# Performance work log

Hardware: AMD Instinct MI355X
Metric: run time of the kernel (lower is better)

Reference implementation:

```python
import jax, jax.numpy as jnp
import numpy as np

N_NODES = 100000
N_EDGES = 1600000
FEAT = 128
HID = 128
N_GRAPHS = 128


def setup_inputs() -> dict:
    key = jax.random.key(0)
    ks = jax.random.split(key, 20)
    inp = {
        'x': jax.random.normal(ks[0], (N_NODES, FEAT), dtype=jnp.float32),
        'edge_index': jax.random.randint(ks[1], (2, N_EDGES), 0, N_NODES, dtype=jnp.int32),
        'batch': jnp.sort(jax.random.randint(ks[2], (N_NODES,), 0, N_GRAPHS, dtype=jnp.int32)),
        'layer_K': 1,
    }
    # Xavier-uniform weights, zero biases (matches LinearPrune.reset_parameters)
    i = 3
    for l in range(3):
        in_dim = FEAT if l == 0 else HID
        lim1 = float(np.sqrt(6.0 / (in_dim + HID)))
        lim2 = float(np.sqrt(6.0 / (HID + HID)))
        inp[f'W1_l{l}'] = jax.random.uniform(ks[i], (HID, in_dim), jnp.float32, -lim1, lim1); i += 1
        inp[f'b1_l{l}'] = jnp.zeros((HID,), jnp.float32)
        inp[f'W2_l{l}'] = jax.random.uniform(ks[i], (HID, HID), jnp.float32, -lim2, lim2); i += 1
        inp[f'b2_l{l}'] = jnp.zeros((HID,), jnp.float32)
    return inp


def _gin_conv(x, src, dst, W1, b1, W2, b2, k):
    # GINConvPrune.forward with skip=1, eps=0, prune=False
    out = x
    for _ in range(k):  # k = layer_K, static int (deterministic finetune/eval path)
        # propagate: gather neighbor feats then scatter-add at dst nodes
        agg = jax.ops.segment_sum(out[src], dst, num_segments=x.shape[0])
        out = (out + agg) * 0.5
    if k == 0:
        out = jax.ops.segment_sum(x[src], dst, num_segments=x.shape[0])
    out = out + x  # (1 + eps) * x_r with eps = 0
    h = jax.nn.relu(out @ W1.T + b1)
    return h @ W2.T + b2


def reference(x, edge_index, batch, layer_K,
              W1_l0, b1_l0, W2_l0, b2_l0,
              W1_l1, b1_l1, W2_l1, b2_l1,
              W1_l2, b1_l2, W2_l2, b2_l2):
    src, dst = edge_index[0], edge_index[1]
    params = [(W1_l0, b1_l0, W2_l0, b2_l0),
              (W1_l1, b1_l1, W2_l1, b2_l1),
              (W1_l2, b1_l2, W2_l2, b2_l2)]
    k = int(layer_K)
    h = x
    pooled = []
    for (W1, b1, W2, b2) in params:
        h = _gin_conv(h, src, dst, W1, b1, W2, b2, k)
        h = jax.nn.relu(h)  # outer self.act
        pooled.append(jax.ops.segment_sum(h, batch, num_segments=N_GRAPHS))  # global_add_pool
    return jnp.concatenate(pooled, axis=1)  # [G, 3*HID]
```

## Files before the change

kernel.cpp:

```cpp
#include <hip/hip_runtime.h>

#define NN 100000
#define NE 1600000
#define FEAT 128
#define NGRAPH 128
#define BSHIFT 9
#define NB 196
#define NCHUNK 400
#define CHUNK 4000

typedef __attribute__((ext_vector_type(8))) short bf16x8;
typedef __attribute__((ext_vector_type(4))) float f32x4;
typedef __attribute__((ext_vector_type(4))) unsigned u32x4;

union U4 { u32x4 u; bf16x8 v; };

__device__ __forceinline__ unsigned short f2bf(float f) {
    unsigned u = __float_as_uint(f);
    return (unsigned short)((u + 0x7fffu + ((u >> 16) & 1u)) >> 16);
}
__device__ __forceinline__ float bf2f(unsigned short h) {
    return __uint_as_float(((unsigned)h) << 16);
}
__device__ __forceinline__ unsigned packbf(float f) {
    unsigned short h = f2bf(f);
    return (unsigned)h | ((unsigned)f2bf(f - bf2f(h)) << 16);
}
__device__ __forceinline__ uint2 unpack2(unsigned p0, unsigned p1) {
    return make_uint2((p0 & 0xffffu) | (p1 << 16), (p0 >> 16) | (p1 & 0xffff0000u));
}
__device__ __forceinline__ void unpack8(u32x4 a, u32x4 b, bf16x8& hv, bf16x8& lv) {
    uint2 r0 = unpack2(a.x, a.y), r1 = unpack2(a.z, a.w);
    uint2 r2 = unpack2(b.x, b.y), r3 = unpack2(b.z, b.w);
    U4 h, l;
    h.u = (u32x4){r0.x, r1.x, r2.x, r3.x};
    l.u = (u32x4){r0.y, r1.y, r2.y, r3.y};
    hv = h.v; lv = l.v;
}

__global__ __launch_bounds__(256)
void wsplit_frag_kernel(const float* __restrict__ W, short* __restrict__ Wf)
{
    int i = blockIdx.x * 256 + threadIdx.x;
    int o = i >> 7, k = i & 127;
    float f = W[i];
    unsigned short h = f2bf(f);
    short lo = (short)f2bf(f - bf2f(h));
    int ct = o >> 4, lr = o & 15, kc = k >> 5, q = (k >> 3) & 3, j = k & 7;
    int idx = (kc * 8 + ct) * 512 + ((q << 4) | lr) * 8 + j;
    Wf[idx] = (short)h;
    Wf[16384 + idx] = lo;
}

__global__ __launch_bounds__(256)
void p1a_count(const int* __restrict__ ei, int* __restrict__ cnt_T)
{
    __shared__ int hist[NB];
    const int b = blockIdx.x, tid = threadIdx.x;
    for (int i = tid; i < NB; i += 256) hist[i] = 0;
    __syncthreads();
    const int e0 = b * CHUNK;
    for (int e = e0 + tid; e < e0 + CHUNK; e += 256)
        atomicAdd(&hist[ei[NE + e] >> BSHIFT], 1);
    __syncthreads();
    for (int k = tid; k < NB; k += 256) cnt_T[k * NCHUNK + b] = hist[k];
}

__global__ __launch_bounds__(1024)
void scan1_kernel(const int* __restrict__ in, int* __restrict__ out,
                  int* __restrict__ bsum, int n)
{
    __shared__ int sh[1024];
    const int tid = threadIdx.x;
    const int gid = blockIdx.x * 1024 + tid;
    int v = (gid < n) ? in[gid] : 0;
    sh[tid] = v;
    __syncthreads();
    #pragma unroll
    for (int d = 1; d < 1024; d <<= 1) {
        int t = (tid >= d) ? sh[tid - d] : 0;
        __syncthreads();
        sh[tid] += t;
        __syncthreads();
    }
    if (gid < n) out[gid] = sh[tid] - v;
    if (tid == 1023) bsum[blockIdx.x] = sh[1023];
}

__global__ __launch_bounds__(128)
void scan2_kernel(int* __restrict__ bsum, int nb)
{
    __shared__ int sh[128];
    const int tid = threadIdx.x;
    int v = (tid < nb) ? bsum[tid] : 0;
    sh[tid] = v;
    __syncthreads();
    #pragma unroll
    for (int d = 1; d < 128; d <<= 1) {
        int t = (tid >= d) ? sh[tid - d] : 0;
        __syncthreads();
        sh[tid] += t;
        __syncthreads();
    }
    if (tid < nb) bsum[tid] = sh[tid] - v;
}

__global__ __launch_bounds__(1024)
void scan3g_kernel(int* __restrict__ arr, const int* __restrict__ bsum, int n)
{
    const int gid = blockIdx.x * 1024 + threadIdx.x;
    if (gid < n) arr[gid] += bsum[blockIdx.x];
}

__global__ __launch_bounds__(256)
void p1b_scatter(const int* __restrict__ ei, const int* __restrict__ offs_T,
                 int2* __restrict__ ebuf)
{
    __shared__ int cur[NB];
    const int b = blockIdx.x, tid = threadIdx.x;
    for (int i = tid; i < NB; i += 256) cur[i] = offs_T[i * NCHUNK + b];
    __syncthreads();
    const int e0 = b * CHUNK;
    for (int e = e0 + tid; e < e0 + CHUNK; e += 256) {
        int s = ei[e], d = ei[NE + e];
        int pos = atomicAdd(&cur[d >> BSHIFT], 1);
        ebuf[pos] = make_int2(s, d);
    }
}

__global__ __launch_bounds__(512)
void p2_csr(const int2* __restrict__ ebuf, const int* __restrict__ offs_T,
            int* __restrict__ off, int* __restrict__ csr)
{
    __shared__ int degc[512];
    __shared__ int sh[512];
    const int k = blockIdx.x, tid = threadIdx.x;
    const int base = k << BSHIFT;
    const int bs = offs_T[k * NCHUNK];
    const int be = (k == NB - 1) ? NE : offs_T[(k + 1) * NCHUNK];
    degc[tid] = 0;
    __syncthreads();
    for (int e = bs + tid; e < be; e += 512)
        atomicAdd(&degc[ebuf[e].y - base], 1);
    __syncthreads();
    int v = degc[tid];
    sh[tid] = v;
    __syncthreads();
    #pragma unroll
    for (int d = 1; d < 512; d <<= 1) {
        int t = (tid >= d) ? sh[tid - d] : 0;
        __syncthreads();
        sh[tid] += t;
        __syncthreads();
    }
    const int excl = bs + sh[tid] - v;
    const int n = base + tid;
    if (n <= NN) off[n] = excl;
    degc[tid] = excl;
    __syncthreads();
    for (int e = bs + tid; e < be; e += 512) {
        int2 p = ebuf[e];
        int slot = atomicAdd(&degc[p.y - base], 1);
        csr[slot] = p.x;
    }
}

__global__ __launch_bounds__(256)
void aggregate_pack_kernel(const float* __restrict__ h, const int* __restrict__ off,
                           const int* __restrict__ csr, unsigned* __restrict__ xP, int nn)
{
    const int node = blockIdx.x * 4 + (threadIdx.x >> 6);
    if (node >= nn) return;
    const int lane = threadIdx.x & 63;
    const int s = off[node], e = off[node + 1];
    float2 acc = make_float2(0.f, 0.f);
    for (int base = s; base < e; base += 64) {
        const int cnt = min(64, e - base);
        int src_l = (base + lane < e) ? csr[base + lane] : 0;
        for (int jb = 0; jb < cnt; jb += 16) {
            float2 v[16];
            #pragma unroll
            for (int q = 0; q < 16; ++q) {
                int sq = __shfl(src_l, (jb + q) & 63);
                v[q] = reinterpret_cast<const float2*>(h + (size_t)sq * FEAT)[lane];
            }
            #pragma unroll
            for (int q = 0; q < 16; ++q) {
                if (jb + q < cnt) { acc.x += v[q].x; acc.y += v[q].y; }
            }
        }
    }
    float2 hv = reinterpret_cast<const float2*>(h + (size_t)node * FEAT)[lane];
    float ox = (hv.x + acc.x) * 0.5f + hv.x;
    float oy = (hv.y + acc.y) * 0.5f + hv.y;
    uint2 pw = make_uint2(packbf(ox), packbf(oy));
    *reinterpret_cast<uint2*>(&xP[(size_t)node * FEAT + lane * 2]) = pw;
}

__global__ __launch_bounds__(512, 4)
void layer_fused_kernel(const unsigned* __restrict__ aP, const short* __restrict__ Wf1,
                        const short* __restrict__ Wf2, const float* __restrict__ b1,
                        const float* __restrict__ b2, float* __restrict__ outC, int n_nodes)
{
    __shared__ short wlds[32768];
    const int tid = threadIdx.x;
    const int lane = tid & 63;
    const int w = tid >> 6;
    const int lr = lane & 15;
    const int lq = lane >> 4;
    const int n0 = blockIdx.x * 128 + w * 16 + lr;
    const bool v0 = (n0 < n_nodes);
    const size_t rb0 = (size_t)n0 * FEAT + lq * 8;
    u32x4 zz = {};

    {
        const bf16x8* src = reinterpret_cast<const bf16x8*>(Wf1);
        bf16x8* dst = reinterpret_cast<bf16x8*>(wlds);
        #pragma unroll
        for (int it = 0; it < 8; ++it)
            dst[it * 512 + tid] = src[it * 512 + tid];
    }
    u32x4 paa = v0 ? *reinterpret_cast<const u32x4*>(&aP[rb0])     : zz;
    u32x4 pab = v0 ? *reinterpret_cast<const u32x4*>(&aP[rb0 + 4]) : zz;
    __syncthreads();

    f32x4 acc[8] = {};
    bf16x8 ah, al;
    unpack8(paa, pab, ah, al);
    #pragma unroll
    for (int kc = 0; kc < 4; ++kc) {
        u32x4 na = zz, nb = zz;
        if (kc < 3) {
            const int ko = (kc + 1) * 32;
            na = v0 ? *reinterpret_cast<const u32x4*>(&aP[rb0 + ko])     : zz;
            nb = v0 ? *reinterpret_cast<const u32x4*>(&aP[rb0 + ko + 4]) : zz;
        }
        #pragma unroll
        for (int ct = 0; ct < 8; ++ct) {
            const int ra = (kc * 8 + ct) * 512 + lane * 8;
            bf16x8 bh = *reinterpret_cast<const bf16x8*>(&wlds[ra]);
            bf16x8 bl = *reinterpret_cast<const bf16x8*>(&wlds[16384 + ra]);
            acc[ct] = __builtin_amdgcn_mfma_f32_16x16x32_bf16(bh, ah, acc[ct], 0, 0, 0);
            acc[ct] = __builtin_amdgcn_mfma_f32_16x16x32_bf16(bh, al, acc[ct], 0, 0, 0);
            acc[ct] = __builtin_amdgcn_mfma_f32_16x16x32_bf16(bl, ah, acc[ct], 0, 0, 0);
        }
        if (kc < 3) unpack8(na, nb, ah, al);
    }

    unsigned h1p[32];
    #pragma unroll
    for (int ct = 0; ct < 8; ++ct) {
        const int c0 = ct * 16 + lq * 4;
        float4 bv = *reinterpret_cast<const float4*>(&b1[c0]);
        h1p[ct * 4 + 0] = packbf(fmaxf(acc[ct][0] + bv.x, 0.f));
        h1p[ct * 4 + 1] = packbf(fmaxf(acc[ct][1] + bv.y, 0.f));
        h1p[ct * 4 + 2] = packbf(fmaxf(acc[ct][2] + bv.z, 0.f));
        h1p[ct * 4 + 3] = packbf(fmaxf(acc[ct][3] + bv.w, 0.f));
    }

    __syncthreads();
    {
        const bf16x8* src = reinterpret_cast<const bf16x8*>(Wf2);
        bf16x8* dst = reinterpret_cast<bf16x8*>(wlds);
        #pragma unroll
        for (int it = 0; it < 8; ++it)
            dst[it * 512 + tid] = src[it * 512 + tid];
    }
    __syncthreads();

    f32x4 acc2[8] = {};
    const int aown = (lq & 1) * 2;
    const bool hi_t = (lq & 2) != 0;
    #pragma unroll
    for (int kc = 0; kc < 4; ++kc) {
        unsigned pd[8];
        #pragma unroll
        for (int m = 0; m < 4; ++m) {
            unsigned vA = h1p[(2 * kc) * 4 + m];
            unsigned vB = h1p[(2 * kc + 1) * 4 + m];
            unsigned sA0 = __shfl(vA, lr + 16 * aown);
            unsigned sB0 = __shfl(vB, lr + 16 * aown);
            unsigned sA1 = __shfl(vA, lr + 16 * (aown + 1));
            unsigned sB1 = __shfl(vB, lr + 16 * (aown + 1));
            pd[m]     = hi_t ? sB0 : sA0;
            pd[4 + m] = hi_t ? sB1 : sA1;
        }
        u32x4 qa = {pd[0], pd[1], pd[2], pd[3]};
        u32x4 qb = {pd[4], pd[5], pd[6], pd[7]};
        bf16x8 hh, hl;
        unpack8(qa, qb, hh, hl);
        #pragma unroll
        for (int ct = 0; ct < 8; ++ct) {
            const int ra = (kc * 8 + ct) * 512 + lane * 8;
            bf16x8 bh = *reinterpret_cast<const bf16x8*>(&wlds[ra]);
            bf16x8 bl = *reinterpret_cast<const bf16x8*>(&wlds[16384 + ra]);
            acc2[ct] = __builtin_amdgcn_mfma_f32_16x16x32_bf16(bh, hh, acc2[ct], 0, 0, 0);
            acc2[ct] = __builtin_amdgcn_mfma_f32_16x16x32_bf16(bh, hl, acc2[ct], 0, 0, 0);
            acc2[ct] = __builtin_amdgcn_mfma_f32_16x16x32_bf16(bl, hh, acc2[ct], 0, 0, 0);
        }
    }

    if (v0) {
        #pragma unroll
        for (int ct = 0; ct < 8; ++ct) {
            const int c0 = ct * 16 + lq * 4;
            float4 bv = *reinterpret_cast<const float4*>(&b2[c0]);
            float4 o;
            o.x = fmaxf(acc2[ct][0] + bv.x, 0.f);
            o.y = fmaxf(acc2[ct][1] + bv.y, 0.f);
            o.z = fmaxf(acc2[ct][2] + bv.z, 0.f);
            o.w = fmaxf(acc2[ct][3] + bv.w, 0.f);
            *reinterpret_cast<float4*>(&outC[(size_t)n0 * FEAT + c0]) = o;
        }
    }
}

__global__ __launch_bounds__(512)
void pool_kernel(const float* __restrict__ y, const int* __restrict__ batch,
                 float* __restrict__ out, int n_nodes, int layer)
{
    const int g = blockIdx.x;
    int lo = 0, hi = n_nodes;
    while (lo < hi) { int mid = (lo + hi) >> 1; if (batch[mid] < g) lo = mid + 1; else hi = mid; }
    const int start = lo;
    hi = n_nodes;
    while (lo < hi) { int mid = (lo + hi) >> 1; if (batch[mid] < g + 1) lo = mid + 1; else hi = mid; }
    const int end = lo;

    const int tid = threadIdx.x;
    const int f = tid & 127;
    const int q = tid >> 7;
    float sum = 0.f;
    for (int n = start + q; n < end; n += 4)
        sum += y[(size_t)n * FEAT + f];

    __shared__ float red[512];
    red[tid] = sum;
    __syncthreads();
    if (tid < 128)
        out[g * (3 * FEAT) + layer * FEAT + tid]
            = red[tid] + red[tid + 128] + red[tid + 256] + red[tid + 384];
}

__global__ __launch_bounds__(256)
void scatter_kernel(const float* __restrict__ h, const int* __restrict__ ei,
                    float* __restrict__ agg, int n_edges)
{
    int e = blockIdx.x * 4 + (threadIdx.x >> 6);
    if (e >= n_edges) return;
    int lane = threadIdx.x & 63;
    int s = ei[e];
    int d = ei[n_edges + e];
    float2 v = reinterpret_cast<const float2*>(h + (size_t)s * FEAT)[lane];
    float* ap = agg + (size_t)d * FEAT + lane * 2;
    atomicAdd(ap, v.x);
    atomicAdd(ap + 1, v.y);
}

__global__ __launch_bounds__(256)
void combine_kernel(const float* __restrict__ h, float* __restrict__ agg_xeff, size_t n4)
{
    size_t i = (size_t)blockIdx.x * 256 + threadIdx.x;
    if (i >= n4) return;
    float4 a = reinterpret_cast<const float4*>(h)[i];
    float4 g = reinterpret_cast<float4*>(agg_xeff)[i];
    float4 o;
    o.x = (a.x + g.x) * 0.5f + a.x;
    o.y = (a.y + g.y) * 0.5f + a.y;
    o.z = (a.z + g.z) * 0.5f + a.z;
    o.w = (a.w + g.w) * 0.5f + a.w;
    reinterpret_cast<float4*>(agg_xeff)[i] = o;
}

__global__ __launch_bounds__(256, 2)
void gemm_relu_kernel(const float* __restrict__ A, const float* __restrict__ W,
                      const float* __restrict__ bias, float* __restrict__ out, int n_nodes)
{
    __shared__ float xt[64][128];
    __shared__ float wt[64][128];
    const int tid = threadIdx.x;
    const int row0 = blockIdx.x * 128;
    const int r  = tid >> 1;
    const int ks = (tid & 1) << 5;
    const int tn = (tid >> 4) << 3;
    const int to = (tid & 15) << 3;
    float acc[8][8] = {};

    for (int c = 0; c < 2; ++c) {
        const int k0 = c * 64;
        {
            const float4* wrow = reinterpret_cast<const float4*>(W + r * FEAT + k0 + ks);
            #pragma unroll
            for (int i = 0; i < 8; ++i) {
                float4 w4 = wrow[i];
                int kk = ks + i * 4;
                wt[kk + 0][r] = w4.x; wt[kk + 1][r] = w4.y;
                wt[kk + 2][r] = w4.z; wt[kk + 3][r] = w4.w;
            }
        }
        {
            const int n = row0 + r;
            if (n < n_nodes) {
                const float4* ar = reinterpret_cast<const float4*>(A + (size_t)n * FEAT + k0 + ks);
                #pragma unroll
                for (int i = 0; i < 8; ++i) {
                    float4 a4 = ar[i];
                    int kk = ks + i * 4;
                    xt[kk + 0][r] = a4.x; xt[kk + 1][r] = a4.y;
                    xt[kk + 2][r] = a4.z; xt[kk + 3][r] = a4.w;
                }
            } else {
                #pragma unroll
                for (int i = 0; i < 8; ++i) {
                    int kk = ks + i * 4;
                    xt[kk + 0][r] = 0.f; xt[kk + 1][r] = 0.f;
                    xt[kk + 2][r] = 0.f; xt[kk + 3][r] = 0.f;
                }
            }
        }
        __syncthreads();
        #pragma unroll 4
        for (int k = 0; k < 64; ++k) {
            float4 x0 = *reinterpret_cast<const float4*>(&xt[k][tn]);
            float4 x1 = *reinterpret_cast<const float4*>(&xt[k][tn + 4]);
            float4 w0 = *reinterpret_cast<const float4*>(&wt[k][to]);
            float4 w1 = *reinterpret_cast<const float4*>(&wt[k][to + 4]);
            float xv[8] = {x0.x, x0.y, x0.z, x0.w, x1.x, x1.y, x1.z, x1.w};
            float wv[8] = {w0.x, w0.y, w0.z, w0.w, w1.x, w1.y, w1.z, w1.w};
            #pragma unroll
            for (int i = 0; i < 8; ++i)
                #pragma unroll
                for (int j = 0; j < 8; ++j)
                    acc[i][j] = fmaf(xv[i], wv[j], acc[i][j]);
        }
        __syncthreads();
    }

    float bv[8];
    #pragma unroll
    for (int j = 0; j < 8; ++j) bv[j] = bias[to + j];
    #pragma unroll
    for (int i = 0; i < 8; ++i) {
        int n = row0 + tn + i;
        if (n >= n_nodes) break;
        float4 o0, o1;
        o0.x = fmaxf(acc[i][0] + bv[0], 0.f);
        o0.y = fmaxf(acc[i][1] + bv[1], 0.f);
        o0.z = fmaxf(acc[i][2] + bv[2], 0.f);
        o0.w = fmaxf(acc[i][3] + bv[3], 0.f);
        o1.x = fmaxf(acc[i][4] + bv[4], 0.f);
        o1.y = fmaxf(acc[i][5] + bv[5], 0.f);
        o1.z = fmaxf(acc[i][6] + bv[6], 0.f);
        o1.w = fmaxf(acc[i][7] + bv[7], 0.f);
        float* op = out + (size_t)n * FEAT + to;
        *reinterpret_cast<float4*>(op) = o0;
        *reinterpret_cast<float4*>(op + 4) = o1;
    }
}

extern "C" void kernel_launch(void* const* d_in, const int* in_sizes, int n_in,
                              void* d_out, int out_size, void* d_ws, size_t ws_size,
                              hipStream_t stream)
{
    const float* x     = (const float*)d_in[0];
    const int*   ei    = (const int*)d_in[1];
    const int*   batch = (const int*)d_in[2];
    const float* W1[3] = {(const float*)d_in[4], (const float*)d_in[8],  (const float*)d_in[12]};
    const float* b1[3] = {(const float*)d_in[5], (const float*)d_in[9],  (const float*)d_in[13]};
    const float* W2[3] = {(const float*)d_in[6], (const float*)d_in[10], (const float*)d_in[14]};
    const float* b2[3] = {(const float*)d_in[7], (const float*)d_in[11], (const float*)d_in[15]};

    const size_t nf = (size_t)NN * FEAT;
    float* outp = (float*)d_out;
    const int fused_grid = (NN + 127) / 128;
    const int M = NB * NCHUNK;
    const int scanM_blocks = (M + 1023) / 1024;
    const int WN = FEAT * FEAT;

    const size_t need_full = 2 * nf * 4 + (size_t)(NN + 1 + NE) * 4 + (size_t)12 * WN * 2;

    if (ws_size >= need_full) {
        unsigned* xeffP = (unsigned*)d_ws;
        float* bufC     = (float*)(xeffP + nf);
        int* off        = (int*)(bufC + nf);
        int* csr        = off + (NN + 1);
        short* wbase    = (short*)(csr + NE);
        short* wf[6];
        for (int i = 0; i < 6; ++i) wf[i] = wbase + (size_t)i * 2 * WN;
        int* cnt_T  = (int*)xeffP;
        int* offs_T = cnt_T + M;
        int* bsum   = offs_T + M;
        int2* ebuf  = (int2*)bufC;

        const float* Ws[6] = {W1[0], W2[0], W1[1], W2[1], W1[2], W2[2]};
        for (int i = 0; i < 6; ++i)
            wsplit_frag_kernel<<<WN / 256, 256, 0, stream>>>(Ws[i], wf[i]);

        p1a_count<<<NCHUNK, 256, 0, stream>>>(ei, cnt_T);
        scan1_kernel<<<scanM_blocks, 1024, 0, stream>>>(cnt_T, offs_T, bsum, M);
        scan2_kernel<<<1, 128, 0, stream>>>(bsum, scanM_blocks);
        scan3g_kernel<<<scanM_blocks, 1024, 0, stream>>>(offs_T, bsum, M);
        p1b_scatter<<<NCHUNK, 256, 0, stream>>>(ei, offs_T, ebuf);
        p2_csr<<<NB, 512, 0, stream>>>(ebuf, offs_T, off, csr);

        const float* h = x;
        for (int l = 0; l < 3; ++l) {
            aggregate_pack_kernel<<<(NN + 3) / 4, 256, 0, stream>>>(h, off, csr, xeffP, NN);
            layer_fused_kernel<<<fused_grid, 512, 0, stream>>>(xeffP, wf[2 * l], wf[2 * l + 1],
                                                               b1[l], b2[l], bufC, NN);
            pool_kernel<<<NGRAPH, 512, 0, stream>>>(bufC, batch, outp, NN, l);
            h = bufC;
        }
    } else if (ws_size >= 3 * nf * 4) {
        float* bufA = (float*)d_ws;
        float* bufB = bufA + nf;
        float* bufC = bufB + nf;
        const int gg = (NN + 127) / 128;
        const float* h = x;
        for (int l = 0; l < 3; ++l) {
            hipMemsetAsync(bufA, 0, nf * 4, stream);
            scatter_kernel<<<(NE + 3) / 4, 256, 0, stream>>>(h, ei, bufA, NE);
            combine_kernel<<<(int)((nf / 4 + 255) / 256), 256, 0, stream>>>(h, bufA, nf / 4);
            gemm_relu_kernel<<<gg, 256, 0, stream>>>(bufA, W1[l], b1[l], bufB, NN);
            gemm_relu_kernel<<<gg, 256, 0, stream>>>(bufB, W2[l], b2[l], bufC, NN);
            pool_kernel<<<NGRAPH, 512, 0, stream>>>(bufC, batch, outp, NN, l);
            h = bufC;
        }
    }
}
```

Baseline: 692.2 us.

## Fuse neighbor aggregation into the per-layer MLP kernel with ping-pong output buffers

Removes the separate aggregation kernel and does the CSR gather-sum inside the fused MLP kernel. Each wave aggregates its 16 rows one after another and shuffles the bf16-packed results straight into the MFMA A-operand registers. This drops the intermediate bf16 write and read and one launch per layer. Because the kernel now reads h while writing its output, the output alternates between two buffers, and the workspace layout moves to fit them. The cost is that each wave handles its 16 rows' gathers serially with fewer waves in flight (512-thread blocks at 128 rows each), which may hurt latency hiding for the memory-bound gather.

```diff
diff --git a/kernel.cpp b/kernel.cpp
--- a/kernel.cpp
+++ b/kernel.cpp
@@ -165,42 +165,12 @@
     }
 }
 
-__global__ __launch_bounds__(256)
-void aggregate_pack_kernel(const float* __restrict__ h, const int* __restrict__ off,
-                           const int* __restrict__ csr, unsigned* __restrict__ xP, int nn)
-{
-    const int node = blockIdx.x * 4 + (threadIdx.x >> 6);
-    if (node >= nn) return;
-    const int lane = threadIdx.x & 63;
-    const int s = off[node], e = off[node + 1];
-    float2 acc = make_float2(0.f, 0.f);
-    for (int base = s; base < e; base += 64) {
-        const int cnt = min(64, e - base);
-        int src_l = (base + lane < e) ? csr[base + lane] : 0;
-        for (int jb = 0; jb < cnt; jb += 16) {
-            float2 v[16];
-            #pragma unroll
-            for (int q = 0; q < 16; ++q) {
-                int sq = __shfl(src_l, (jb + q) & 63);
-                v[q] = reinterpret_cast<const float2*>(h + (size_t)sq * FEAT)[lane];
-            }
-            #pragma unroll
-            for (int q = 0; q < 16; ++q) {
-                if (jb + q < cnt) { acc.x += v[q].x; acc.y += v[q].y; }
-            }
-        }
-    }
-    float2 hv = reinterpret_cast<const float2*>(h + (size_t)node * FEAT)[lane];
-    float ox = (hv.x + acc.x) * 0.5f + hv.x;
-    float oy = (hv.y + acc.y) * 0.5f + hv.y;
-    uint2 pw = make_uint2(packbf(ox), packbf(oy));
-    *reinterpret_cast<uint2*>(&xP[(size_t)node * FEAT + lane * 2]) = pw;
-}
-
 __global__ __launch_bounds__(512, 4)
-void layer_fused_kernel(const unsigned* __restrict__ aP, const short* __restrict__ Wf1,
-                        const short* __restrict__ Wf2, const float* __restrict__ b1,
-                        const float* __restrict__ b2, float* __restrict__ outC, int n_nodes)
+void layer_mega_kernel(const float* __restrict__ h, const int* __restrict__ off,
+                       const int* __restrict__ csr,
+                       const short* __restrict__ Wf1, const short* __restrict__ Wf2,
+                       const float* __restrict__ b1, const float* __restrict__ b2,
+                       float* __restrict__ outC, int n_nodes)
 {
     __shared__ short wlds[32768];
     const int tid = threadIdx.x;
@@ -208,10 +178,7 @@
     const int w = tid >> 6;
     const int lr = lane & 15;
     const int lq = lane >> 4;
-    const int n0 = blockIdx.x * 128 + w * 16 + lr;
-    const bool v0 = (n0 < n_nodes);
-    const size_t rb0 = (size_t)n0 * FEAT + lq * 8;
-    u32x4 zz = {};
+    const int rowbase = blockIdx.x * 128 + w * 16;
 
     {
         const bf16x8* src = reinterpret_cast<const bf16x8*>(Wf1);
@@ -220,31 +187,66 @@
         for (int it = 0; it < 8; ++it)
             dst[it * 512 + tid] = src[it * 512 + tid];
     }
-    u32x4 paa = v0 ? *reinterpret_cast<const u32x4*>(&aP[rb0])     : zz;
-    u32x4 pab = v0 ? *reinterpret_cast<const u32x4*>(&aP[rb0 + 4]) : zz;
-    __syncthreads();
-
-    f32x4 acc[8] = {};
-    bf16x8 ah, al;
-    unpack8(paa, pab, ah, al);
+
+    unsigned areg[32] = {};
+    #pragma unroll
+    for (int r = 0; r < 16; ++r) {
+        const int row = rowbase + r;
+        float2 acc = make_float2(0.f, 0.f);
+        if (row < n_nodes) {
+            const int s = off[row], e = off[row + 1];
+            for (int base = s; base < e; base += 64) {
+                const int cnt = min(64, e - base);
+                int src_l = (base + lane < e) ? csr[base + lane] : 0;
+                for (int jb = 0; jb < cnt; jb += 16) {
+                    float2 v[16];
+                    #pragma unroll
+                    for (int q = 0; q < 16; ++q) {
+                        int sq = __shfl(src_l, (jb + q) & 63);
+                        v[q] = reinterpret_cast<const float2*>(h + (size_t)sq * FEAT)[lane];
+                    }
+                    #pragma unroll
+                    for (int q = 0; q < 16; ++q)
+                        if (jb + q < cnt) { acc.x += v[q].x; acc.y += v[q].y; }
+                }
+            }
+            float2 hv = reinterpret_cast<const float2*>(h + (size_t)row * FEAT)[lane];
+            acc.x = (hv.x + acc.x) * 0.5f + hv.x;
+            acc.y = (hv.y + acc.y) * 0.5f + hv.y;
+        }
+        unsigned px = packbf(acc.x), py = packbf(acc.y);
+        #pragma unroll
+        for (int kc = 0; kc < 4; ++kc) {
+            #pragma unroll
+            for (int t = 0; t < 4; ++t) {
+                const int srcl = kc * 16 + lq * 4 + t;
+                unsigned sx = __shfl(px, srcl);
+                unsigned sy = __shfl(py, srcl);
+                if (lr == r) {
+                    areg[kc * 8 + 2 * t]     = sx;
+                    areg[kc * 8 + 2 * t + 1] = sy;
+                }
+            }
+        }
+    }
+    __syncthreads();
+
+    f32x4 acc1[8] = {};
     #pragma unroll
     for (int kc = 0; kc < 4; ++kc) {
-        u32x4 na = zz, nb = zz;
-        if (kc < 3) {
-            const int ko = (kc + 1) * 32;
-            na = v0 ? *reinterpret_cast<const u32x4*>(&aP[rb0 + ko])     : zz;
-            nb = v0 ? *reinterpret_cast<const u32x4*>(&aP[rb0 + ko + 4]) : zz;
-        }
+        u32x4 qa = {areg[kc * 8 + 0], areg[kc * 8 + 1], areg[kc * 8 + 2], areg[kc * 8 + 3]};
+        u32x4 qb = {areg[kc * 8 + 4], areg[kc * 8 + 5], areg[kc * 8 + 6], areg[kc * 8 + 7]};
+        bf16x8 ah, al;
+        unpack8(qa, qb, ah, al);
         #pragma unroll
         for (int ct = 0; ct < 8; ++ct) {
             const int ra = (kc * 8 + ct) * 512 + lane * 8;
             bf16x8 bh = *reinterpret_cast<const bf16x8*>(&wlds[ra]);
             bf16x8 bl = *reinterpret_cast<const bf16x8*>(&wlds[16384 + ra]);
-            acc[ct] = __builtin_amdgcn_mfma_f32_16x16x32_bf16(bh, ah, acc[ct], 0, 0, 0);
-            acc[ct] = __builtin_amdgcn_mfma_f32_16x16x32_bf16(bh, al, acc[ct], 0, 0, 0);
-            acc[ct] = __builtin_amdgcn_mfma_f32_16x16x32_bf16(bl, ah, acc[ct], 0, 0, 0);
-        }
-        if (kc < 3) unpack8(na, nb, ah, al);
+            acc1[ct] = __builtin_amdgcn_mfma_f32_16x16x32_bf16(bh, ah, acc1[ct], 0, 0, 0);
+            acc1[ct] = __builtin_amdgcn_mfma_f32_16x16x32_bf16(bh, al, acc1[ct], 0, 0, 0);
+            acc1[ct] = __builtin_amdgcn_mfma_f32_16x16x32_bf16(bl, ah, acc1[ct], 0, 0, 0);
+        }
     }
 
     unsigned h1p[32];
@@ -252,10 +254,10 @@
     for (int ct = 0; ct < 8; ++ct) {
         const int c0 = ct * 16 + lq * 4;
         float4 bv = *reinterpret_cast<const float4*>(&b1[c0]);
-        h1p[ct * 4 + 0] = packbf(fmaxf(acc[ct][0] + bv.x, 0.f));
-        h1p[ct * 4 + 1] = packbf(fmaxf(acc[ct][1] + bv.y, 0.f));
-        h1p[ct * 4 + 2] = packbf(fmaxf(acc[ct][2] + bv.z, 0.f));
-        h1p[ct * 4 + 3] = packbf(fmaxf(acc[ct][3] + bv.w, 0.f));
+        h1p[ct * 4 + 0] = packbf(fmaxf(acc1[ct][0] + bv.x, 0.f));
+        h1p[ct * 4 + 1] = packbf(fmaxf(acc1[ct][1] + bv.y, 0.f));
+        h1p[ct * 4 + 2] = packbf(fmaxf(acc1[ct][2] + bv.z, 0.f));
+        h1p[ct * 4 + 3] = packbf(fmaxf(acc1[ct][3] + bv.w, 0.f));
     }
 
     __syncthreads();
@@ -300,7 +302,8 @@
         }
     }
 
-    if (v0) {
+    const int n0 = rowbase + lr;
+    if (n0 < n_nodes) {
         #pragma unroll
         for (int ct = 0; ct < 8; ++ct) {
             const int c0 = ct * 16 + lq * 4;
@@ -472,7 +475,7 @@
 
     const size_t nf = (size_t)NN * FEAT;
     float* outp = (float*)d_out;
-    const int fused_grid = (NN + 127) / 128;
+    const int mega_grid = (NN + 127) / 128;
     const int M = NB * NCHUNK;
     const int scanM_blocks = (M + 1023) / 1024;
     const int WN = FEAT * FEAT;
@@ -480,17 +483,17 @@
     const size_t need_full = 2 * nf * 4 + (size_t)(NN + 1 + NE) * 4 + (size_t)12 * WN * 2;
 
     if (ws_size >= need_full) {
-        unsigned* xeffP = (unsigned*)d_ws;
-        float* bufC     = (float*)(xeffP + nf);
-        int* off        = (int*)(bufC + nf);
-        int* csr        = off + (NN + 1);
-        short* wbase    = (short*)(csr + NE);
+        float* bufC  = (float*)d_ws;
+        float* bufD  = bufC + nf;
+        int* off     = (int*)(bufD + nf);
+        int* csr     = off + (NN + 1);
+        short* wbase = (short*)(csr + NE);
         short* wf[6];
         for (int i = 0; i < 6; ++i) wf[i] = wbase + (size_t)i * 2 * WN;
-        int* cnt_T  = (int*)xeffP;
+        int2* ebuf  = (int2*)bufD;
+        int* cnt_T  = (int*)(ebuf + NE);
         int* offs_T = cnt_T + M;
         int* bsum   = offs_T + M;
-        int2* ebuf  = (int2*)bufC;
 
         const float* Ws[6] = {W1[0], W2[0], W1[1], W2[1], W1[2], W2[2]};
         for (int i = 0; i < 6; ++i)
@@ -504,12 +507,13 @@
         p2_csr<<<NB, 512, 0, stream>>>(ebuf, offs_T, off, csr);
 
         const float* h = x;
+        float* bufs[2] = {bufC, bufD};
         for (int l = 0; l < 3; ++l) {
-            aggregate_pack_kernel<<<(NN + 3) / 4, 256, 0, stream>>>(h, off, csr, xeffP, NN);
-            layer_fused_kernel<<<fused_grid, 512, 0, stream>>>(xeffP, wf[2 * l], wf[2 * l + 1],
-                                                               b1[l], b2[l], bufC, NN);
-            pool_kernel<<<NGRAPH, 512, 0, stream>>>(bufC, batch, outp, NN, l);
-            h = bufC;
+            float* out_l = bufs[l & 1];
+            layer_mega_kernel<<<mega_grid, 512, 0, stream>>>(h, off, csr, wf[2 * l], wf[2 * l + 1],
+                                                             b1[l], b2[l], out_l, NN);
+            pool_kernel<<<NGRAPH, 512, 0, stream>>>(out_l, batch, outp, NN, l);
+            h = out_l;
         }
     } else if (ws_size >= 3 * nf * 4) {
         float* bufA = (float*)d_ws;
```

Measured after the change: 2.308 ms. 234% more time.
